# Performance work log

Hardware: AMD Instinct MI355X
Metric: run time of the kernel (lower is better)

## Reference

```python
import jax, jax.numpy as jnp
import numpy as np

TOP_K = 8


def setup_inputs() -> dict:
    key = jax.random.key(0)
    k1, k2, k3, k4, k5 = jax.random.split(key, 5)
    B, S, H, E, I = 1, 2048, 2048, 32, 768
    return {
        "hidden_states": jax.random.normal(k1, (B, S, H), dtype=jnp.float32),
        "gate_w": jax.random.normal(k2, (E, H), dtype=jnp.float32) * (H ** -0.5),
        "w_gate_proj": jax.random.normal(k3, (E, I, H), dtype=jnp.float32) * (H ** -0.5),
        "w_up_proj": jax.random.normal(k4, (E, I, H), dtype=jnp.float32) * (H ** -0.5),
        "w_down_proj": jax.random.normal(k5, (E, H, I), dtype=jnp.float32) * (I ** -0.5),
    }


def _masked_routing(router_logits):
    # norm_topk_prob=True branch: topk logits -> softmax over the k selected
    T, E = router_logits.shape
    sel_w, sel_e = jax.lax.top_k(router_logits, TOP_K)          # [T,k]
    sel_w = jax.nn.softmax(sel_w.astype(jnp.float32), axis=1)    # [T,k]
    rows = jnp.arange(T)[:, None]
    masked = jnp.zeros((T, E), dtype=jnp.float32).at[rows, sel_e].set(sel_w)
    count = jnp.zeros((E,), dtype=jnp.int32).at[sel_e.reshape(-1)].add(1)
    return masked, count


def reference(hidden_states, gate_w, w_gate_proj, w_up_proj, w_down_proj):
    B, S, H = hidden_states.shape
    x = hidden_states.reshape(-1, H)                              # [T,H]
    router_logits = x @ gate_w.T                                  # [T,E]
    masked_w, _count = _masked_routing(router_logits)
    # custom_moe_glu: per-expert GLU MLP, combined with masked routing weights
    g = jnp.einsum("th,eih->tei", x, w_gate_proj)                # [T,E,I]
    u = jnp.einsum("th,eih->tei", x, w_up_proj)                  # [T,E,I]
    h = jax.nn.silu(g) * u                                        # [T,E,I]
    h = h * masked_w[:, :, None]                                  # zero unselected experts
    out = jnp.einsum("tei,ehi->th", h, w_down_proj)              # [T,H]
    return out.reshape(B, S, H)
```

## Files before the change

### kernel.cpp

```cpp
#include <hip/hip_runtime.h>

#define T_TOK 2048
#define H_DIM 2048
#define E_NUM 32
#define I_DIM 768
#define TOPK 8

typedef __attribute__((ext_vector_type(8))) _Float16 f16x8;
typedef __attribute__((ext_vector_type(4))) _Float16 f16x4;
typedef __attribute__((ext_vector_type(4))) float f32x4;

__global__ __launch_bounds__(256) void cvt_x_kernel(const float* __restrict__ x,
                                                    _Float16* __restrict__ xh) {
    int i = blockIdx.x * 256 + threadIdx.x;
    f32x4 f = ((const f32x4*)x)[i];
    f16x4 h;
    h[0] = (_Float16)f[0]; h[1] = (_Float16)f[1];
    h[2] = (_Float16)f[2]; h[3] = (_Float16)f[3];
    ((f16x4*)xh)[i] = h;
}

__global__ __launch_bounds__(256) void router_kernel(const float* __restrict__ x,
                                                     const float* __restrict__ gw,
                                                     int* __restrict__ sel_e,
                                                     float* __restrict__ sel_w,
                                                     int* __restrict__ counts) {
    int t = blockIdx.x;
    int tid = threadIdx.x, lane = tid & 63, wave = tid >> 6;
    __shared__ float logits[E_NUM];
    const float* xr = x + (size_t)t * H_DIM;
    float xv[32];
#pragma unroll
    for (int c = 0; c < 32; ++c) xv[c] = xr[lane + c * 64];
    for (int j = 0; j < 8; ++j) {
        int e = wave * 8 + j;
        const float* wr = gw + (size_t)e * H_DIM;
        float acc = 0.f;
#pragma unroll
        for (int c = 0; c < 32; ++c) acc += xv[c] * wr[lane + c * 64];
#pragma unroll
        for (int s = 32; s > 0; s >>= 1) acc += __shfl_xor(acc, s, 64);
        if (lane == 0) logits[e] = acc;
    }
    __syncthreads();
    if (tid == 0) {
        float lg[E_NUM];
        for (int e2 = 0; e2 < E_NUM; ++e2) lg[e2] = logits[e2];
        unsigned taken = 0;
        float sv[TOPK]; int se[TOPK];
        for (int k = 0; k < TOPK; ++k) {
            float best = -3.4e38f; int bi = 0;
            for (int e2 = 0; e2 < E_NUM; ++e2)
                if (!((taken >> e2) & 1u) && lg[e2] > best) { best = lg[e2]; bi = e2; }
            taken |= 1u << bi; sv[k] = best; se[k] = bi;
        }
        float m = sv[0], s = 0.f;
        for (int k = 0; k < TOPK; ++k) { sv[k] = expf(sv[k] - m); s += sv[k]; }
        float inv = 1.f / s;
        for (int k = 0; k < TOPK; ++k) {
            sel_e[t * TOPK + k] = se[k];
            sel_w[t * TOPK + k] = sv[k] * inv;
            atomicAdd(&counts[se[k]], 1);
        }
    }
}

__global__ void scan_kernel(const int* __restrict__ counts, int* __restrict__ offs) {
    if (threadIdx.x == 0) {
        int s = 0;
        for (int e = 0; e < E_NUM; ++e) { offs[e] = s; s += counts[e]; }
        offs[E_NUM] = s;
    }
}

__global__ __launch_bounds__(256) void scatter_kernel(const int* __restrict__ sel_e,
                                                      const float* __restrict__ sel_w,
                                                      const int* __restrict__ offs,
                                                      int* __restrict__ cursor,
                                                      int* __restrict__ pair_token,
                                                      float* __restrict__ pair_w) {
    int t = blockIdx.x * 256 + threadIdx.x;
    if (t >= T_TOK) return;
    for (int k = 0; k < TOPK; ++k) {
        int e = sel_e[t * TOPK + k];
        int pos = atomicAdd(&cursor[e], 1);
        int slot = offs[e] + pos;
        pair_token[slot] = t;
        pair_w[slot] = sel_w[t * TOPK + k];
    }
}

__global__ __launch_bounds__(256, 2) void mlp1_kernel(const _Float16* __restrict__ xh,
                                                      const float* __restrict__ wg,
                                                      const float* __restrict__ wu,
                                                      const int* __restrict__ offs,
                                                      const int* __restrict__ pair_token,
                                                      const float* __restrict__ pair_w,
                                                      _Float16* __restrict__ h_buf) {
    int e = blockIdx.z, mt = blockIdx.y, nt = blockIdx.x;
    int base = offs[e], cnt = offs[e + 1] - base;
    if (mt * 128 >= cnt) return;
    int tid = threadIdx.x, lane = tid & 63, wave = tid >> 6;

    __shared__ _Float16 As[128 * 40];
    __shared__ _Float16 Bg[128 * 40];
    __shared__ _Float16 Bu[128 * 40];

    const _Float16* aSrc[2]; int aDst[2];
#pragma unroll
    for (int i = 0; i < 2; ++i) {
        int c = tid + i * 256;
        int row = c >> 2, col8 = c & 3;
        int g = mt * 128 + row;
        int tok = (g < cnt) ? pair_token[base + g] : pair_token[base];
        aSrc[i] = xh + (size_t)tok * H_DIM + col8 * 8;
        aDst[i] = row * 40 + col8 * 8;
    }
    const float* gSrc[4]; const float* uSrc[4]; int bDst[4];
#pragma unroll
    for (int i = 0; i < 4; ++i) {
        int c = tid + i * 256;
        int row = c >> 3, col4 = c & 7;
        size_t wOff = ((size_t)e * I_DIM + nt * 128 + row) * H_DIM + col4 * 4;
        gSrc[i] = wg + wOff; uSrc[i] = wu + wOff;
        bDst[i] = row * 40 + col4 * 4;
    }

    const f32x4 zero = {0.f, 0.f, 0.f, 0.f};
    f32x4 accg[4][4], accu[4][4];
#pragma unroll
    for (int mi = 0; mi < 4; ++mi)
#pragma unroll
        for (int ni = 0; ni < 4; ++ni) { accg[mi][ni] = zero; accu[mi][ni] = zero; }

    int m16 = lane & 15, quad = lane >> 4, wm = wave >> 1, wn = wave & 1;

    for (int k0 = 0; k0 < H_DIM; k0 += 32) {
#pragma unroll
        for (int i = 0; i < 2; ++i)
            *(f16x8*)&As[aDst[i]] = *(const f16x8*)(aSrc[i] + k0);
#pragma unroll
        for (int i = 0; i < 4; ++i) {
            f32x4 fg = *(const f32x4*)(gSrc[i] + k0);
            f32x4 fu = *(const f32x4*)(uSrc[i] + k0);
            f16x4 hg, hu;
#pragma unroll
            for (int q = 0; q < 4; ++q) { hg[q] = (_Float16)fg[q]; hu[q] = (_Float16)fu[q]; }
            *(f16x4*)&Bg[bDst[i]] = hg;
            *(f16x4*)&Bu[bDst[i]] = hu;
        }
        __syncthreads();
        f16x8 a[4], bg[4], bu[4];
#pragma unroll
        for (int mi = 0; mi < 4; ++mi)
            a[mi] = *(const f16x8*)&As[(wm * 64 + mi * 16 + m16) * 40 + quad * 8];
#pragma unroll
        for (int ni = 0; ni < 4; ++ni) {
            int r = (wn * 64 + ni * 16 + m16) * 40 + quad * 8;
            bg[ni] = *(const f16x8*)&Bg[r];
            bu[ni] = *(const f16x8*)&Bu[r];
        }
#pragma unroll
        for (int mi = 0; mi < 4; ++mi)
#pragma unroll
            for (int ni = 0; ni < 4; ++ni) {
                accg[mi][ni] = __builtin_amdgcn_mfma_f32_16x16x32_f16(a[mi], bg[ni], accg[mi][ni], 0, 0, 0);
                accu[mi][ni] = __builtin_amdgcn_mfma_f32_16x16x32_f16(a[mi], bu[ni], accu[mi][ni], 0, 0, 0);
            }
        __syncthreads();
    }

#pragma unroll
    for (int mi = 0; mi < 4; ++mi) {
#pragma unroll
        for (int reg = 0; reg < 4; ++reg) {
            int rloc = wm * 64 + mi * 16 + quad * 4 + reg;
            int g = mt * 128 + rloc;
            if (g >= cnt) continue;
            int slot = base + g;
            float pw = pair_w[slot];
#pragma unroll
            for (int ni = 0; ni < 4; ++ni) {
                int col = nt * 128 + wn * 64 + ni * 16 + m16;
                float gv = accg[mi][ni][reg];
                float uv = accu[mi][ni][reg];
                float hv = (gv / (1.f + expf(-gv))) * uv * pw;
                h_buf[(size_t)slot * I_DIM + col] = (_Float16)hv;
            }
        }
    }
}

__global__ __launch_bounds__(256, 2) void mlp2_kernel(const _Float16* __restrict__ h_buf,
                                                      const float* __restrict__ wd,
                                                      const int* __restrict__ offs,
                                                      const int* __restrict__ pair_token,
                                                      float* __restrict__ out) {
    int e = blockIdx.z, mt = blockIdx.y, nt = blockIdx.x;
    int base = offs[e], cnt = offs[e + 1] - base;
    if (mt * 128 >= cnt) return;
    int tid = threadIdx.x, lane = tid & 63, wave = tid >> 6;

    __shared__ _Float16 As[128 * 40];
    __shared__ _Float16 Bs[128 * 40];

    const _Float16* aSrc[2]; int aDst[2];
#pragma unroll
    for (int i = 0; i < 2; ++i) {
        int c = tid + i * 256;
        int row = c >> 2, col8 = c & 3;
        int g = mt * 128 + row;
        int slot = (g < cnt) ? (base + g) : base;
        aSrc[i] = h_buf + (size_t)slot * I_DIM + col8 * 8;
        aDst[i] = row * 40 + col8 * 8;
    }
    const float* bSrc[4]; int bDst[4];
#pragma unroll
    for (int i = 0; i < 4; ++i) {
        int c = tid + i * 256;
        int row = c >> 3, col4 = c & 7;
        bSrc[i] = wd + ((size_t)e * H_DIM + nt * 128 + row) * I_DIM + col4 * 4;
        bDst[i] = row * 40 + col4 * 4;
    }

    const f32x4 zero = {0.f, 0.f, 0.f, 0.f};
    f32x4 acc[4][4];
#pragma unroll
    for (int mi = 0; mi < 4; ++mi)
#pragma unroll
        for (int ni = 0; ni < 4; ++ni) acc[mi][ni] = zero;

    int m16 = lane & 15, quad = lane >> 4, wm = wave >> 1, wn = wave & 1;

    for (int k0 = 0; k0 < I_DIM; k0 += 32) {
#pragma unroll
        for (int i = 0; i < 2; ++i)
            *(f16x8*)&As[aDst[i]] = *(const f16x8*)(aSrc[i] + k0);
#pragma unroll
        for (int i = 0; i < 4; ++i) {
            f32x4 f = *(const f32x4*)(bSrc[i] + k0);
            f16x4 h;
#pragma unroll
            for (int q = 0; q < 4; ++q) h[q] = (_Float16)f[q];
            *(f16x4*)&Bs[bDst[i]] = h;
        }
        __syncthreads();
        f16x8 a[4], b[4];
#pragma unroll
        for (int mi = 0; mi < 4; ++mi)
            a[mi] = *(const f16x8*)&As[(wm * 64 + mi * 16 + m16) * 40 + quad * 8];
#pragma unroll
        for (int ni = 0; ni < 4; ++ni)
            b[ni] = *(const f16x8*)&Bs[(wn * 64 + ni * 16 + m16) * 40 + quad * 8];
#pragma unroll
        for (int mi = 0; mi < 4; ++mi)
#pragma unroll
            for (int ni = 0; ni < 4; ++ni)
                acc[mi][ni] = __builtin_amdgcn_mfma_f32_16x16x32_f16(a[mi], b[ni], acc[mi][ni], 0, 0, 0);
        __syncthreads();
    }

#pragma unroll
    for (int mi = 0; mi < 4; ++mi) {
#pragma unroll
        for (int reg = 0; reg < 4; ++reg) {
            int rloc = wm * 64 + mi * 16 + quad * 4 + reg;
            int g = mt * 128 + rloc;
            if (g >= cnt) continue;
            int t = pair_token[base + g];
#pragma unroll
            for (int ni = 0; ni < 4; ++ni) {
                int col = nt * 128 + wn * 64 + ni * 16 + m16;
                atomicAdd(&out[(size_t)t * H_DIM + col], acc[mi][ni][reg]);
            }
        }
    }
}

extern "C" void kernel_launch(void* const* d_in, const int* in_sizes, int n_in,
                              void* d_out, int out_size, void* d_ws, size_t ws_size,
                              hipStream_t stream) {
    const float* x  = (const float*)d_in[0];
    const float* gw = (const float*)d_in[1];
    const float* wg = (const float*)d_in[2];
    const float* wu = (const float*)d_in[3];
    const float* wd = (const float*)d_in[4];
    float* out = (float*)d_out;

    char* ws = (char*)d_ws;
    int*      sel_e      = (int*)(ws + 0);
    float*    sel_w      = (float*)(ws + 65536);
    int*      counts     = (int*)(ws + 131072);
    int*      cursor     = (int*)(ws + 131200);
    int*      offs       = (int*)(ws + 131328);
    int*      pair_token = (int*)(ws + 131584);
    float*    pair_w     = (float*)(ws + 197120);
    _Float16* xh         = (_Float16*)(ws + 262656);
    _Float16* h_buf      = (_Float16*)(ws + 8651264);

    hipMemsetAsync(ws + 131072, 0, 256, stream);
    hipMemsetAsync(d_out, 0, (size_t)T_TOK * H_DIM * sizeof(float), stream);

    cvt_x_kernel<<<(T_TOK * H_DIM / 4) / 256, 256, 0, stream>>>(x, xh);
    router_kernel<<<T_TOK, 256, 0, stream>>>(x, gw, sel_e, sel_w, counts);
    scan_kernel<<<1, 64, 0, stream>>>(counts, offs);
    scatter_kernel<<<T_TOK / 256, 256, 0, stream>>>(sel_e, sel_w, offs, cursor, pair_token, pair_w);
    mlp1_kernel<<<dim3(6, 16, 32), 256, 0, stream>>>(xh, wg, wu, offs, pair_token, pair_w, h_buf);
    mlp2_kernel<<<dim3(16, 16, 32), 256, 0, stream>>>(h_buf, wd, offs, pair_token, out);
}
```

Baseline: 959.5 us.

## Retile MoE GEMMs to 256-row tiles, add register prefetch and XCD-aware block mapping

```diff
diff --git a/kernel.cpp b/kernel.cpp
--- a/kernel.cpp
+++ b/kernel.cpp
@@ -90,6 +90,8 @@
     }
 }
 
+#define M1_MT 8
+#define M1_NT 12
 __global__ __launch_bounds__(256, 2) void mlp1_kernel(const _Float16* __restrict__ xh,
                                                       const float* __restrict__ wg,
                                                       const float* __restrict__ wu,
@@ -97,31 +99,35 @@
                                                       const int* __restrict__ pair_token,
                                                       const float* __restrict__ pair_w,
                                                       _Float16* __restrict__ h_buf) {
-    int e = blockIdx.z, mt = blockIdx.y, nt = blockIdx.x;
+    int b = blockIdx.x;
+    int lid = (b & 7) * (M1_MT * M1_NT * E_NUM / 8) + (b >> 3);
+    int mt = lid & 7;
+    int nt = (lid >> 3) % M1_NT;
+    int e  = (lid >> 3) / M1_NT;
     int base = offs[e], cnt = offs[e + 1] - base;
-    if (mt * 128 >= cnt) return;
+    if (mt * 256 >= cnt) return;
     int tid = threadIdx.x, lane = tid & 63, wave = tid >> 6;
 
-    __shared__ _Float16 As[128 * 40];
-    __shared__ _Float16 Bg[128 * 40];
-    __shared__ _Float16 Bu[128 * 40];
-
-    const _Float16* aSrc[2]; int aDst[2];
-#pragma unroll
-    for (int i = 0; i < 2; ++i) {
+    __shared__ _Float16 As[256 * 40];
+    __shared__ _Float16 Bg[64 * 40];
+    __shared__ _Float16 Bu[64 * 40];
+
+    const _Float16* aSrc[4]; int aDst[4];
+#pragma unroll
+    for (int i = 0; i < 4; ++i) {
         int c = tid + i * 256;
         int row = c >> 2, col8 = c & 3;
-        int g = mt * 128 + row;
+        int g = mt * 256 + row;
         int tok = (g < cnt) ? pair_token[base + g] : pair_token[base];
         aSrc[i] = xh + (size_t)tok * H_DIM + col8 * 8;
         aDst[i] = row * 40 + col8 * 8;
     }
-    const float* gSrc[4]; const float* uSrc[4]; int bDst[4];
-#pragma unroll
-    for (int i = 0; i < 4; ++i) {
+    const float* gSrc[2]; const float* uSrc[2]; int bDst[2];
+#pragma unroll
+    for (int i = 0; i < 2; ++i) {
         int c = tid + i * 256;
         int row = c >> 3, col4 = c & 7;
-        size_t wOff = ((size_t)e * I_DIM + nt * 128 + row) * H_DIM + col4 * 4;
+        size_t wOff = ((size_t)e * I_DIM + nt * 64 + row) * H_DIM + col4 * 4;
         gSrc[i] = wg + wOff; uSrc[i] = wu + wOff;
         bDst[i] = row * 40 + col4 * 4;
     }
@@ -133,30 +139,41 @@
 #pragma unroll
         for (int ni = 0; ni < 4; ++ni) { accg[mi][ni] = zero; accu[mi][ni] = zero; }
 
-    int m16 = lane & 15, quad = lane >> 4, wm = wave >> 1, wn = wave & 1;
+    int m16 = lane & 15, quad = lane >> 4;
+
+    f16x8 aReg[4]; f32x4 gReg[2], uReg[2];
+#pragma unroll
+    for (int i = 0; i < 4; ++i) aReg[i] = *(const f16x8*)(aSrc[i]);
+#pragma unroll
+    for (int i = 0; i < 2; ++i) { gReg[i] = *(const f32x4*)(gSrc[i]); uReg[i] = *(const f32x4*)(uSrc[i]); }
 
     for (int k0 = 0; k0 < H_DIM; k0 += 32) {
 #pragma unroll
-        for (int i = 0; i < 2; ++i)
-            *(f16x8*)&As[aDst[i]] = *(const f16x8*)(aSrc[i] + k0);
-#pragma unroll
-        for (int i = 0; i < 4; ++i) {
-            f32x4 fg = *(const f32x4*)(gSrc[i] + k0);
-            f32x4 fu = *(const f32x4*)(uSrc[i] + k0);
+        for (int i = 0; i < 4; ++i)
+            *(f16x8*)&As[aDst[i]] = aReg[i];
+#pragma unroll
+        for (int i = 0; i < 2; ++i) {
             f16x4 hg, hu;
 #pragma unroll
-            for (int q = 0; q < 4; ++q) { hg[q] = (_Float16)fg[q]; hu[q] = (_Float16)fu[q]; }
+            for (int q = 0; q < 4; ++q) { hg[q] = (_Float16)gReg[i][q]; hu[q] = (_Float16)uReg[i][q]; }
             *(f16x4*)&Bg[bDst[i]] = hg;
             *(f16x4*)&Bu[bDst[i]] = hu;
         }
         __syncthreads();
+        if (k0 + 32 < H_DIM) {
+            int kn = k0 + 32;
+#pragma unroll
+            for (int i = 0; i < 4; ++i) aReg[i] = *(const f16x8*)(aSrc[i] + kn);
+#pragma unroll
+            for (int i = 0; i < 2; ++i) { gReg[i] = *(const f32x4*)(gSrc[i] + kn); uReg[i] = *(const f32x4*)(uSrc[i] + kn); }
+        }
         f16x8 a[4], bg[4], bu[4];
 #pragma unroll
         for (int mi = 0; mi < 4; ++mi)
-            a[mi] = *(const f16x8*)&As[(wm * 64 + mi * 16 + m16) * 40 + quad * 8];
+            a[mi] = *(const f16x8*)&As[(wave * 64 + mi * 16 + m16) * 40 + quad * 8];
 #pragma unroll
         for (int ni = 0; ni < 4; ++ni) {
-            int r = (wn * 64 + ni * 16 + m16) * 40 + quad * 8;
+            int r = (ni * 16 + m16) * 40 + quad * 8;
             bg[ni] = *(const f16x8*)&Bg[r];
             bu[ni] = *(const f16x8*)&Bu[r];
         }
@@ -174,14 +191,14 @@
     for (int mi = 0; mi < 4; ++mi) {
 #pragma unroll
         for (int reg = 0; reg < 4; ++reg) {
-            int rloc = wm * 64 + mi * 16 + quad * 4 + reg;
-            int g = mt * 128 + rloc;
+            int rloc = wave * 64 + mi * 16 + quad * 4 + reg;
+            int g = mt * 256 + rloc;
             if (g >= cnt) continue;
             int slot = base + g;
             float pw = pair_w[slot];
 #pragma unroll
             for (int ni = 0; ni < 4; ++ni) {
-                int col = nt * 128 + wn * 64 + ni * 16 + m16;
+                int col = nt * 64 + ni * 16 + m16;
                 float gv = accg[mi][ni][reg];
                 float uv = accu[mi][ni][reg];
                 float hv = (gv / (1.f + expf(-gv))) * uv * pw;
@@ -191,25 +208,31 @@
     }
 }
 
+#define M2_MT 8
+#define M2_NT 16
 __global__ __launch_bounds__(256, 2) void mlp2_kernel(const _Float16* __restrict__ h_buf,
                                                       const float* __restrict__ wd,
                                                       const int* __restrict__ offs,
                                                       const int* __restrict__ pair_token,
                                                       float* __restrict__ out) {
-    int e = blockIdx.z, mt = blockIdx.y, nt = blockIdx.x;
+    int b = blockIdx.x;
+    int lid = (b & 7) * (M2_MT * M2_NT * E_NUM / 8) + (b >> 3);
+    int mt = lid & 7;
+    int nt = (lid >> 3) & 15;
+    int e  = lid >> 7;
     int base = offs[e], cnt = offs[e + 1] - base;
-    if (mt * 128 >= cnt) return;
+    if (mt * 256 >= cnt) return;
     int tid = threadIdx.x, lane = tid & 63, wave = tid >> 6;
 
-    __shared__ _Float16 As[128 * 40];
+    __shared__ _Float16 As[256 * 40];
     __shared__ _Float16 Bs[128 * 40];
 
-    const _Float16* aSrc[2]; int aDst[2];
-#pragma unroll
-    for (int i = 0; i < 2; ++i) {
+    const _Float16* aSrc[4]; int aDst[4];
+#pragma unroll
+    for (int i = 0; i < 4; ++i) {
         int c = tid + i * 256;
         int row = c >> 2, col8 = c & 3;
-        int g = mt * 128 + row;
+        int g = mt * 256 + row;
         int slot = (g < cnt) ? (base + g) : base;
         aSrc[i] = h_buf + (size_t)slot * I_DIM + col8 * 8;
         aDst[i] = row * 40 + col8 * 8;
@@ -224,39 +247,47 @@
     }
 
     const f32x4 zero = {0.f, 0.f, 0.f, 0.f};
-    f32x4 acc[4][4];
+    f32x4 acc[4][8];
 #pragma unroll
     for (int mi = 0; mi < 4; ++mi)
 #pragma unroll
-        for (int ni = 0; ni < 4; ++ni) acc[mi][ni] = zero;
-
-    int m16 = lane & 15, quad = lane >> 4, wm = wave >> 1, wn = wave & 1;
+        for (int ni = 0; ni < 8; ++ni) acc[mi][ni] = zero;
+
+    int m16 = lane & 15, quad = lane >> 4;
+
+    f16x8 aReg[4]; f32x4 bReg[4];
+#pragma unroll
+    for (int i = 0; i < 4; ++i) { aReg[i] = *(const f16x8*)(aSrc[i]); bReg[i] = *(const f32x4*)(bSrc[i]); }
 
     for (int k0 = 0; k0 < I_DIM; k0 += 32) {
 #pragma unroll
-        for (int i = 0; i < 2; ++i)
-            *(f16x8*)&As[aDst[i]] = *(const f16x8*)(aSrc[i] + k0);
+        for (int i = 0; i < 4; ++i)
+            *(f16x8*)&As[aDst[i]] = aReg[i];
 #pragma unroll
         for (int i = 0; i < 4; ++i) {
-            f32x4 f = *(const f32x4*)(bSrc[i] + k0);
             f16x4 h;
 #pragma unroll
-            for (int q = 0; q < 4; ++q) h[q] = (_Float16)f[q];
+            for (int q = 0; q < 4; ++q) h[q] = (_Float16)bReg[i][q];
             *(f16x4*)&Bs[bDst[i]] = h;
         }
         __syncthreads();
-        f16x8 a[4], b[4];
+        if (k0 + 32 < I_DIM) {
+            int kn = k0 + 32;
+#pragma unroll
+            for (int i = 0; i < 4; ++i) { aReg[i] = *(const f16x8*)(aSrc[i] + kn); bReg[i] = *(const f32x4*)(bSrc[i] + kn); }
+        }
+        f16x8 a[4], bb[8];
 #pragma unroll
         for (int mi = 0; mi < 4; ++mi)
-            a[mi] = *(const f16x8*)&As[(wm * 64 + mi * 16 + m16) * 40 + quad * 8];
-#pragma unroll
-        for (int ni = 0; ni < 4; ++ni)
-            b[ni] = *(const f16x8*)&Bs[(wn * 64 + ni * 16 + m16) * 40 + quad * 8];
+            a[mi] = *(const f16x8*)&As[(wave * 64 + mi * 16 + m16) * 40 + quad * 8];
+#pragma unroll
+        for (int ni = 0; ni < 8; ++ni)
+            bb[ni] = *(const f16x8*)&Bs[(ni * 16 + m16) * 40 + quad * 8];
 #pragma unroll
         for (int mi = 0; mi < 4; ++mi)
 #pragma unroll
-            for (int ni = 0; ni < 4; ++ni)
-                acc[mi][ni] = __builtin_amdgcn_mfma_f32_16x16x32_f16(a[mi], b[ni], acc[mi][ni], 0, 0, 0);
+            for (int ni = 0; ni < 8; ++ni)
+                acc[mi][ni] = __builtin_amdgcn_mfma_f32_16x16x32_f16(a[mi], bb[ni], acc[mi][ni], 0, 0, 0);
         __syncthreads();
     }
 
@@ -264,13 +295,13 @@
     for (int mi = 0; mi < 4; ++mi) {
 #pragma unroll
         for (int reg = 0; reg < 4; ++reg) {
-            int rloc = wm * 64 + mi * 16 + quad * 4 + reg;
-            int g = mt * 128 + rloc;
+            int rloc = wave * 64 + mi * 16 + quad * 4 + reg;
+            int g = mt * 256 + rloc;
             if (g >= cnt) continue;
             int t = pair_token[base + g];
 #pragma unroll
-            for (int ni = 0; ni < 4; ++ni) {
-                int col = nt * 128 + wn * 64 + ni * 16 + m16;
+            for (int ni = 0; ni < 8; ++ni) {
+                int col = nt * 128 + ni * 16 + m16;
                 atomicAdd(&out[(size_t)t * H_DIM + col], acc[mi][ni][reg]);
             }
         }
@@ -305,6 +336,6 @@
     router_kernel<<<T_TOK, 256, 0, stream>>>(x, gw, sel_e, sel_w, counts);
     scan_kernel<<<1, 64, 0, stream>>>(counts, offs);
     scatter_kernel<<<T_TOK / 256, 256, 0, stream>>>(sel_e, sel_w, offs, cursor, pair_token, pair_w);
-    mlp1_kernel<<<dim3(6, 16, 32), 256, 0, stream>>>(xh, wg, wu, offs, pair_token, pair_w, h_buf);
-    mlp2_kernel<<<dim3(16, 16, 32), 256, 0, stream>>>(h_buf, wd, offs, pair_token, out);
-}
+    mlp1_kernel<<<M1_MT * M1_NT * E_NUM, 256, 0, stream>>>(xh, wg, wu, offs, pair_token, pair_w, h_buf);
+    mlp2_kernel<<<M2_MT * M2_NT * E_NUM, 256, 0, stream>>>(h_buf, wd, offs, pair_token, out);
+}
```

New measurement: 1.049 ms. 9.3% more time.

## Double-buffer MoE GEMM tiles, remap blocks per XCD, narrow mlp1 N tile

Applied to the files above, without the earlier changes.

```diff
diff --git a/kernel.cpp b/kernel.cpp
--- a/kernel.cpp
+++ b/kernel.cpp
@@ -90,21 +90,29 @@
     }
 }
 
-__global__ __launch_bounds__(256, 2) void mlp1_kernel(const _Float16* __restrict__ xh,
+#define M1_MT 16
+#define M1_NT 12
+__global__ __launch_bounds__(256, 3) void mlp1_kernel(const _Float16* __restrict__ xh,
                                                       const float* __restrict__ wg,
                                                       const float* __restrict__ wu,
                                                       const int* __restrict__ offs,
                                                       const int* __restrict__ pair_token,
                                                       const float* __restrict__ pair_w,
                                                       _Float16* __restrict__ h_buf) {
-    int e = blockIdx.z, mt = blockIdx.y, nt = blockIdx.x;
+    int b = blockIdx.x;
+    int xcd = b & 7;
+    int j = b >> 3;
+    int mt = j & 15;
+    int slab = (j >> 4) * 8 + xcd;
+    int e = slab / 12;
+    int nt = slab % 12;
     int base = offs[e], cnt = offs[e + 1] - base;
     if (mt * 128 >= cnt) return;
     int tid = threadIdx.x, lane = tid & 63, wave = tid >> 6;
 
-    __shared__ _Float16 As[128 * 40];
-    __shared__ _Float16 Bg[128 * 40];
-    __shared__ _Float16 Bu[128 * 40];
+    __shared__ _Float16 As[2][128 * 40];
+    __shared__ _Float16 Bg[2][64 * 40];
+    __shared__ _Float16 Bu[2][64 * 40];
 
     const _Float16* aSrc[2]; int aDst[2];
 #pragma unroll
@@ -116,58 +124,88 @@
         aSrc[i] = xh + (size_t)tok * H_DIM + col8 * 8;
         aDst[i] = row * 40 + col8 * 8;
     }
-    const float* gSrc[4]; const float* uSrc[4]; int bDst[4];
-#pragma unroll
-    for (int i = 0; i < 4; ++i) {
+    const float* gSrc[2]; const float* uSrc[2]; int bDst[2];
+#pragma unroll
+    for (int i = 0; i < 2; ++i) {
         int c = tid + i * 256;
         int row = c >> 3, col4 = c & 7;
-        size_t wOff = ((size_t)e * I_DIM + nt * 128 + row) * H_DIM + col4 * 4;
+        size_t wOff = ((size_t)e * I_DIM + nt * 64 + row) * H_DIM + col4 * 4;
         gSrc[i] = wg + wOff; uSrc[i] = wu + wOff;
         bDst[i] = row * 40 + col4 * 4;
     }
 
     const f32x4 zero = {0.f, 0.f, 0.f, 0.f};
-    f32x4 accg[4][4], accu[4][4];
+    f32x4 accg[4][2], accu[4][2];
 #pragma unroll
     for (int mi = 0; mi < 4; ++mi)
 #pragma unroll
-        for (int ni = 0; ni < 4; ++ni) { accg[mi][ni] = zero; accu[mi][ni] = zero; }
+        for (int ni = 0; ni < 2; ++ni) { accg[mi][ni] = zero; accu[mi][ni] = zero; }
 
     int m16 = lane & 15, quad = lane >> 4, wm = wave >> 1, wn = wave & 1;
 
+    f16x8 aReg[2]; f32x4 gReg[2], uReg[2];
+#pragma unroll
+    for (int i = 0; i < 2; ++i) aReg[i] = *(const f16x8*)(aSrc[i]);
+#pragma unroll
+    for (int i = 0; i < 2; ++i) { gReg[i] = *(const f32x4*)(gSrc[i]); uReg[i] = *(const f32x4*)(uSrc[i]); }
+
+#pragma unroll
+    for (int i = 0; i < 2; ++i) *(f16x8*)&As[0][aDst[i]] = aReg[i];
+#pragma unroll
+    for (int i = 0; i < 2; ++i) {
+        f16x4 hg, hu;
+#pragma unroll
+        for (int q = 0; q < 4; ++q) { hg[q] = (_Float16)gReg[i][q]; hu[q] = (_Float16)uReg[i][q]; }
+        *(f16x4*)&Bg[0][bDst[i]] = hg;
+        *(f16x4*)&Bu[0][bDst[i]] = hu;
+    }
+    __syncthreads();
+#pragma unroll
+    for (int i = 0; i < 2; ++i) aReg[i] = *(const f16x8*)(aSrc[i] + 32);
+#pragma unroll
+    for (int i = 0; i < 2; ++i) { gReg[i] = *(const f32x4*)(gSrc[i] + 32); uReg[i] = *(const f32x4*)(uSrc[i] + 32); }
+
+    int p = 0;
     for (int k0 = 0; k0 < H_DIM; k0 += 32) {
-#pragma unroll
-        for (int i = 0; i < 2; ++i)
-            *(f16x8*)&As[aDst[i]] = *(const f16x8*)(aSrc[i] + k0);
-#pragma unroll
-        for (int i = 0; i < 4; ++i) {
-            f32x4 fg = *(const f32x4*)(gSrc[i] + k0);
-            f32x4 fu = *(const f32x4*)(uSrc[i] + k0);
-            f16x4 hg, hu;
-#pragma unroll
-            for (int q = 0; q < 4; ++q) { hg[q] = (_Float16)fg[q]; hu[q] = (_Float16)fu[q]; }
-            *(f16x4*)&Bg[bDst[i]] = hg;
-            *(f16x4*)&Bu[bDst[i]] = hu;
-        }
-        __syncthreads();
-        f16x8 a[4], bg[4], bu[4];
+        int nxt = k0 + 32;
+        if (nxt < H_DIM) {
+#pragma unroll
+            for (int i = 0; i < 2; ++i) *(f16x8*)&As[p ^ 1][aDst[i]] = aReg[i];
+#pragma unroll
+            for (int i = 0; i < 2; ++i) {
+                f16x4 hg, hu;
+#pragma unroll
+                for (int q = 0; q < 4; ++q) { hg[q] = (_Float16)gReg[i][q]; hu[q] = (_Float16)uReg[i][q]; }
+                *(f16x4*)&Bg[p ^ 1][bDst[i]] = hg;
+                *(f16x4*)&Bu[p ^ 1][bDst[i]] = hu;
+            }
+            if (nxt + 32 < H_DIM) {
+                int kn = nxt + 32;
+#pragma unroll
+                for (int i = 0; i < 2; ++i) aReg[i] = *(const f16x8*)(aSrc[i] + kn);
+#pragma unroll
+                for (int i = 0; i < 2; ++i) { gReg[i] = *(const f32x4*)(gSrc[i] + kn); uReg[i] = *(const f32x4*)(uSrc[i] + kn); }
+            }
+        }
+        f16x8 a[4], bg[2], bu[2];
 #pragma unroll
         for (int mi = 0; mi < 4; ++mi)
-            a[mi] = *(const f16x8*)&As[(wm * 64 + mi * 16 + m16) * 40 + quad * 8];
-#pragma unroll
-        for (int ni = 0; ni < 4; ++ni) {
-            int r = (wn * 64 + ni * 16 + m16) * 40 + quad * 8;
-            bg[ni] = *(const f16x8*)&Bg[r];
-            bu[ni] = *(const f16x8*)&Bu[r];
+            a[mi] = *(const f16x8*)&As[p][(wm * 64 + mi * 16 + m16) * 40 + quad * 8];
+#pragma unroll
+        for (int ni = 0; ni < 2; ++ni) {
+            int r = (wn * 32 + ni * 16 + m16) * 40 + quad * 8;
+            bg[ni] = *(const f16x8*)&Bg[p][r];
+            bu[ni] = *(const f16x8*)&Bu[p][r];
         }
 #pragma unroll
         for (int mi = 0; mi < 4; ++mi)
 #pragma unroll
-            for (int ni = 0; ni < 4; ++ni) {
+            for (int ni = 0; ni < 2; ++ni) {
                 accg[mi][ni] = __builtin_amdgcn_mfma_f32_16x16x32_f16(a[mi], bg[ni], accg[mi][ni], 0, 0, 0);
                 accu[mi][ni] = __builtin_amdgcn_mfma_f32_16x16x32_f16(a[mi], bu[ni], accu[mi][ni], 0, 0, 0);
             }
         __syncthreads();
+        p ^= 1;
     }
 
 #pragma unroll
@@ -180,8 +218,8 @@
             int slot = base + g;
             float pw = pair_w[slot];
 #pragma unroll
-            for (int ni = 0; ni < 4; ++ni) {
-                int col = nt * 128 + wn * 64 + ni * 16 + m16;
+            for (int ni = 0; ni < 2; ++ni) {
+                int col = nt * 64 + wn * 32 + ni * 16 + m16;
                 float gv = accg[mi][ni][reg];
                 float uv = accu[mi][ni][reg];
                 float hv = (gv / (1.f + expf(-gv))) * uv * pw;
@@ -191,18 +229,26 @@
     }
 }
 
-__global__ __launch_bounds__(256, 2) void mlp2_kernel(const _Float16* __restrict__ h_buf,
+#define M2_MT 16
+#define M2_NT 16
+__global__ __launch_bounds__(256, 3) void mlp2_kernel(const _Float16* __restrict__ h_buf,
                                                       const float* __restrict__ wd,
                                                       const int* __restrict__ offs,
                                                       const int* __restrict__ pair_token,
                                                       float* __restrict__ out) {
-    int e = blockIdx.z, mt = blockIdx.y, nt = blockIdx.x;
+    int b = blockIdx.x;
+    int xcd = b & 7;
+    int j = b >> 3;
+    int mt = j & 15;
+    int slab = (j >> 4) * 8 + xcd;
+    int e = slab >> 4;
+    int nt = slab & 15;
     int base = offs[e], cnt = offs[e + 1] - base;
     if (mt * 128 >= cnt) return;
     int tid = threadIdx.x, lane = tid & 63, wave = tid >> 6;
 
-    __shared__ _Float16 As[128 * 40];
-    __shared__ _Float16 Bs[128 * 40];
+    __shared__ _Float16 As[2][128 * 40];
+    __shared__ _Float16 Bs[2][128 * 40];
 
     const _Float16* aSrc[2]; int aDst[2];
 #pragma unroll
@@ -232,32 +278,62 @@
 
     int m16 = lane & 15, quad = lane >> 4, wm = wave >> 1, wn = wave & 1;
 
+    f16x8 aReg[2]; f32x4 bReg[4];
+#pragma unroll
+    for (int i = 0; i < 2; ++i) aReg[i] = *(const f16x8*)(aSrc[i]);
+#pragma unroll
+    for (int i = 0; i < 4; ++i) bReg[i] = *(const f32x4*)(bSrc[i]);
+
+#pragma unroll
+    for (int i = 0; i < 2; ++i) *(f16x8*)&As[0][aDst[i]] = aReg[i];
+#pragma unroll
+    for (int i = 0; i < 4; ++i) {
+        f16x4 h;
+#pragma unroll
+        for (int q = 0; q < 4; ++q) h[q] = (_Float16)bReg[i][q];
+        *(f16x4*)&Bs[0][bDst[i]] = h;
+    }
+    __syncthreads();
+#pragma unroll
+    for (int i = 0; i < 2; ++i) aReg[i] = *(const f16x8*)(aSrc[i] + 32);
+#pragma unroll
+    for (int i = 0; i < 4; ++i) bReg[i] = *(const f32x4*)(bSrc[i] + 32);
+
+    int p = 0;
     for (int k0 = 0; k0 < I_DIM; k0 += 32) {
-#pragma unroll
-        for (int i = 0; i < 2; ++i)
-            *(f16x8*)&As[aDst[i]] = *(const f16x8*)(aSrc[i] + k0);
-#pragma unroll
-        for (int i = 0; i < 4; ++i) {
-            f32x4 f = *(const f32x4*)(bSrc[i] + k0);
-            f16x4 h;
-#pragma unroll
-            for (int q = 0; q < 4; ++q) h[q] = (_Float16)f[q];
-            *(f16x4*)&Bs[bDst[i]] = h;
-        }
+        int nxt = k0 + 32;
+        if (nxt < I_DIM) {
+#pragma unroll
+            for (int i = 0; i < 2; ++i) *(f16x8*)&As[p ^ 1][aDst[i]] = aReg[i];
+#pragma unroll
+            for (int i = 0; i < 4; ++i) {
+                f16x4 h;
+#pragma unroll
+                for (int q = 0; q < 4; ++q) h[q] = (_Float16)bReg[i][q];
+                *(f16x4*)&Bs[p ^ 1][bDst[i]] = h;
+            }
+            if (nxt + 32 < I_DIM) {
+                int kn = nxt + 32;
+#pragma unroll
+                for (int i = 0; i < 2; ++i) aReg[i] = *(const f16x8*)(aSrc[i] + kn);
+#pragma unroll
+                for (int i = 0; i < 4; ++i) bReg[i] = *(const f32x4*)(bSrc[i] + kn);
+            }
+        }
+        f16x8 a[4], bb[4];
+#pragma unroll
+        for (int mi = 0; mi < 4; ++mi)
+            a[mi] = *(const f16x8*)&As[p][(wm * 64 + mi * 16 + m16) * 40 + quad * 8];
+#pragma unroll
+        for (int ni = 0; ni < 4; ++ni)
+            bb[ni] = *(const f16x8*)&Bs[p][(wn * 64 + ni * 16 + m16) * 40 + quad * 8];
+#pragma unroll
+        for (int mi = 0; mi < 4; ++mi)
+#pragma unroll
+            for (int ni = 0; ni < 4; ++ni)
+                acc[mi][ni] = __builtin_amdgcn_mfma_f32_16x16x32_f16(a[mi], bb[ni], acc[mi][ni], 0, 0, 0);
         __syncthreads();
-        f16x8 a[4], b[4];
-#pragma unroll
-        for (int mi = 0; mi < 4; ++mi)
-            a[mi] = *(const f16x8*)&As[(wm * 64 + mi * 16 + m16) * 40 + quad * 8];
-#pragma unroll
-        for (int ni = 0; ni < 4; ++ni)
-            b[ni] = *(const f16x8*)&Bs[(wn * 64 + ni * 16 + m16) * 40 + quad * 8];
-#pragma unroll
-        for (int mi = 0; mi < 4; ++mi)
-#pragma unroll
-            for (int ni = 0; ni < 4; ++ni)
-                acc[mi][ni] = __builtin_amdgcn_mfma_f32_16x16x32_f16(a[mi], b[ni], acc[mi][ni], 0, 0, 0);
-        __syncthreads();
+        p ^= 1;
     }
 
 #pragma unroll
@@ -305,6 +381,6 @@
     router_kernel<<<T_TOK, 256, 0, stream>>>(x, gw, sel_e, sel_w, counts);
     scan_kernel<<<1, 64, 0, stream>>>(counts, offs);
     scatter_kernel<<<T_TOK / 256, 256, 0, stream>>>(sel_e, sel_w, offs, cursor, pair_token, pair_w);
-    mlp1_kernel<<<dim3(6, 16, 32), 256, 0, stream>>>(xh, wg, wu, offs, pair_token, pair_w, h_buf);
-    mlp2_kernel<<<dim3(16, 16, 32), 256, 0, stream>>>(h_buf, wd, offs, pair_token, out);
-}
+    mlp1_kernel<<<M1_MT * M1_NT * E_NUM, 256, 0, stream>>>(xh, wg, wu, offs, pair_token, pair_w, h_buf);
+    mlp2_kernel<<<M2_MT * M2_NT * E_NUM, 256, 0, stream>>>(h_buf, wd, offs, pair_token, out);
+}
```

Measured after the change: 953.3 us. Within noise of the previous version (-0.7%).
